# Optimization experiments

Measured on AMD Instinct MI355X. Metric: run time of the kernel, lower is better.

The kernel has to match this reference:

```python
import jax, jax.numpy as jnp
import numpy as np

N_NODES = 100000
D = 128
N_ETYPES = 4
E_PER_TYPE = 400000


def setup_inputs() -> dict:
    key = jax.random.key(0)
    k_h, k_src, k_dst, k_w = jax.random.split(key, 4)
    h = jax.random.normal(k_h, (N_NODES, D), dtype=jnp.float32)
    src = jax.random.randint(k_src, (N_ETYPES, E_PER_TYPE), 0, N_NODES, dtype=jnp.int32)
    dst = jax.random.randint(k_dst, (N_ETYPES, E_PER_TYPE), 0, N_NODES, dtype=jnp.int32)
    # Linear(2*D, 1) with xavier_uniform init
    bound = float(np.sqrt(6.0 / (2 * D + 1)))
    W_weight = jax.random.uniform(k_w, (1, 2 * D), dtype=jnp.float32,
                                  minval=-bound, maxval=bound)
    W_bias = jnp.zeros((1,), dtype=jnp.float32)
    return {"h": h, "src": src, "dst": dst, "W_weight": W_weight, "W_bias": W_bias}


def reference(h, src, dst, W_weight, W_bias):
    # Per edge type: gather src/dst node feats, concat, shared Linear(2D->1), sigmoid.
    # cat([h_u, h_v]) @ W.T == h_u @ Wu.T + h_v @ Wv.T (avoids materializing the concat).
    d = h.shape[1]
    Wu = W_weight[:, :d]   # [1, D]
    Wv = W_weight[:, d:]   # [1, D]
    h_u = h[src]           # [T, E, D] gather (irregular access)
    h_v = h[dst]           # [T, E, D]
    score = jnp.einsum('ted,od->teo', h_u, Wu) \
          + jnp.einsum('ted,od->teo', h_v, Wv) + W_bias  # [T, E, 1]
    s = jax.nn.sigmoid(score)
    # scores dict entries are the per-etype slices s[t]; s_l = concat over etypes
    return s.reshape(-1, 1)
```

## Files before the change

kernel.cpp:

```cpp
#include <hip/hip_runtime.h>
#include <math.h>

#define NODES   100000
#define DIM     128
#define NEDGES  1600000

#define LOG2E 1.44269504088896340736f

typedef int   v4i __attribute__((ext_vector_type(4)));
typedef float v4f __attribute__((ext_vector_type(4)));

__global__ __launch_bounds__(256) void node_proj_kernel(
    const float* __restrict__ h,
    const float* __restrict__ W,
    const float* __restrict__ bias_ptr,
    float* __restrict__ pu,
    float* __restrict__ pv,
    int n_nodes)
{
    int tid  = blockIdx.x * blockDim.x + threadIdx.x;
    int lane = tid & 31;
    int node = tid >> 5;
    if (node >= n_nodes) return;

    const v4f hv = __builtin_nontemporal_load(
        reinterpret_cast<const v4f*>(h + (size_t)node * DIM + lane * 4));
    const v4f wu = *reinterpret_cast<const v4f*>(W + lane * 4);
    const v4f wv = *reinterpret_cast<const v4f*>(W + DIM + lane * 4);

    float su = hv.x * wu.x + hv.y * wu.y + hv.z * wu.z + hv.w * wu.w;
    float sv = hv.x * wv.x + hv.y * wv.y + hv.z * wv.z + hv.w * wv.w;

    #pragma unroll
    for (int off = 16; off >= 1; off >>= 1) {
        su += __shfl_xor(su, off);
        sv += __shfl_xor(sv, off);
    }

    if (lane == 0) {
        pu[node] = su;
        pv[node] = sv + bias_ptr[0];
    }
}

__global__ __launch_bounds__(256) void edge_score_kernel(
    const int*   __restrict__ src,
    const int*   __restrict__ dst,
    const float* __restrict__ pu,
    const float* __restrict__ pv,
    float* __restrict__ out,
    int n_quads)
{
    int i = blockIdx.x * blockDim.x + threadIdx.x;
    if (i >= n_quads) return;

    v4i s4 = __builtin_nontemporal_load(reinterpret_cast<const v4i*>(src) + i);
    v4i d4 = __builtin_nontemporal_load(reinterpret_cast<const v4i*>(dst) + i);

    float a0 = pu[s4.x], b0 = pv[d4.x];
    float a1 = pu[s4.y], b1 = pv[d4.y];
    float a2 = pu[s4.z], b2 = pv[d4.z];
    float a3 = pu[s4.w], b3 = pv[d4.w];

    v4f r;
    r.x = a0 + b0;
    r.y = a1 + b1;
    r.z = a2 + b2;
    r.w = a3 + b3;

    r.x = __builtin_amdgcn_rcpf(1.0f + __builtin_amdgcn_exp2f(-r.x * LOG2E));
    r.y = __builtin_amdgcn_rcpf(1.0f + __builtin_amdgcn_exp2f(-r.y * LOG2E));
    r.z = __builtin_amdgcn_rcpf(1.0f + __builtin_amdgcn_exp2f(-r.z * LOG2E));
    r.w = __builtin_amdgcn_rcpf(1.0f + __builtin_amdgcn_exp2f(-r.w * LOG2E));

    __builtin_nontemporal_store(r, reinterpret_cast<v4f*>(out) + i);
}

extern "C" void kernel_launch(void* const* d_in, const int* in_sizes, int n_in,
                              void* d_out, int out_size, void* d_ws, size_t ws_size,
                              hipStream_t stream) {
    const float* h    = (const float*)d_in[0];
    const int*   src  = (const int*)d_in[1];
    const int*   dst  = (const int*)d_in[2];
    const float* W    = (const float*)d_in[3];
    const float* bias = (const float*)d_in[4];
    float* out = (float*)d_out;

    float* pu = (float*)d_ws;
    float* pv = pu + NODES;

    {
        int threads = 256;
        int total   = NODES * 32;
        int blocks  = (total + threads - 1) / threads;
        node_proj_kernel<<<blocks, threads, 0, stream>>>(h, W, bias, pu, pv, NODES);
    }

    {
        int threads = 256;
        int n_quads = NEDGES / 4;
        int blocks  = (n_quads + threads - 1) / threads;
        edge_score_kernel<<<blocks, threads, 0, stream>>>(src, dst, pu, pv, out, n_quads);
    }
}
```

Before: 33.20 us.

## Fuse node projection and edge scoring into one cooperative persistent kernel

Replaces the two kernel launches with a single cooperative kernel of 1024 blocks. Each thread prefetches its src/dst index quads before the node-projection sweep, a grid-wide sync follows, and the edge gathers and sigmoid run afterwards. The aim is to remove the launch gap between kernels and to hide the index-load latency behind the projection work. In exchange it pays for a grid barrier and the cooperative-launch overhead, and it relies on all 1024 blocks being co-resident, which a cooperative launch requires.

```diff
diff --git a/kernel.cpp b/kernel.cpp
--- a/kernel.cpp
+++ b/kernel.cpp
@@ -1,79 +1,101 @@
 #include <hip/hip_runtime.h>
-#include <math.h>
+#include <hip/hip_cooperative_groups.h>
+
+namespace cg = cooperative_groups;
 
 #define NODES   100000
 #define DIM     128
 #define NEDGES  1600000
+#define NQUADS  (NEDGES / 4)
 
 #define LOG2E 1.44269504088896340736f
+
+#define NBLK  1024
+#define NTHR  256
+#define TOTAL (NBLK * NTHR)
+#define NODES_PER_SWEEP (TOTAL / 32)
 
 typedef int   v4i __attribute__((ext_vector_type(4)));
 typedef float v4f __attribute__((ext_vector_type(4)));
 
-__global__ __launch_bounds__(256) void node_proj_kernel(
+__device__ __forceinline__ float fast_sigmoid(float x) {
+    return __builtin_amdgcn_rcpf(1.0f + __builtin_amdgcn_exp2f(-x * LOG2E));
+}
+
+__global__ __launch_bounds__(NTHR, 4) void fused_kernel(
     const float* __restrict__ h,
+    const int*   __restrict__ src,
+    const int*   __restrict__ dst,
     const float* __restrict__ W,
     const float* __restrict__ bias_ptr,
     float* __restrict__ pu,
     float* __restrict__ pv,
-    int n_nodes)
+    float* __restrict__ out)
 {
-    int tid  = blockIdx.x * blockDim.x + threadIdx.x;
-    int lane = tid & 31;
-    int node = tid >> 5;
-    if (node >= n_nodes) return;
+    const int tid  = blockIdx.x * NTHR + threadIdx.x;
+    const int lane = threadIdx.x & 31;
 
-    const v4f hv = __builtin_nontemporal_load(
-        reinterpret_cast<const v4f*>(h + (size_t)node * DIM + lane * 4));
     const v4f wu = *reinterpret_cast<const v4f*>(W + lane * 4);
     const v4f wv = *reinterpret_cast<const v4f*>(W + DIM + lane * 4);
+    const float b = bias_ptr[0];
 
-    float su = hv.x * wu.x + hv.y * wu.y + hv.z * wu.z + hv.w * wu.w;
-    float sv = hv.x * wv.x + hv.y * wv.y + hv.z * wv.z + hv.w * wv.w;
-
-    #pragma unroll
-    for (int off = 16; off >= 1; off >>= 1) {
-        su += __shfl_xor(su, off);
-        sv += __shfl_xor(sv, off);
+    const int i0 = tid;
+    const int i1 = tid + TOTAL;
+    v4i s0_ = __builtin_nontemporal_load(reinterpret_cast<const v4i*>(src) + i0);
+    v4i d0_ = __builtin_nontemporal_load(reinterpret_cast<const v4i*>(dst) + i0);
+    v4i s1_{}, d1_{};
+    const bool has1 = (i1 < NQUADS);
+    if (has1) {
+        s1_ = __builtin_nontemporal_load(reinterpret_cast<const v4i*>(src) + i1);
+        d1_ = __builtin_nontemporal_load(reinterpret_cast<const v4i*>(dst) + i1);
     }
 
-    if (lane == 0) {
-        pu[node] = su;
-        pv[node] = sv + bias_ptr[0];
+    #pragma unroll 2
+    for (int n = tid >> 5; n < NODES; n += NODES_PER_SWEEP) {
+        const v4f hv = __builtin_nontemporal_load(
+            reinterpret_cast<const v4f*>(h + (size_t)n * DIM + lane * 4));
+
+        float su = hv.x * wu.x + hv.y * wu.y + hv.z * wu.z + hv.w * wu.w;
+        float sv = hv.x * wv.x + hv.y * wv.y + hv.z * wv.z + hv.w * wv.w;
+
+        #pragma unroll
+        for (int off = 16; off >= 1; off >>= 1) {
+            su += __shfl_xor(su, off);
+            sv += __shfl_xor(sv, off);
+        }
+
+        if (lane == 0) {
+            pu[n] = su;
+            pv[n] = sv + b;
+        }
     }
-}
 
-__global__ __launch_bounds__(256) void edge_score_kernel(
-    const int*   __restrict__ src,
-    const int*   __restrict__ dst,
-    const float* __restrict__ pu,
-    const float* __restrict__ pv,
-    float* __restrict__ out,
-    int n_quads)
-{
-    int i = blockIdx.x * blockDim.x + threadIdx.x;
-    if (i >= n_quads) return;
+    cg::this_grid().sync();
 
-    v4i s4 = __builtin_nontemporal_load(reinterpret_cast<const v4i*>(src) + i);
-    v4i d4 = __builtin_nontemporal_load(reinterpret_cast<const v4i*>(dst) + i);
-
-    float a0 = pu[s4.x], b0 = pv[d4.x];
-    float a1 = pu[s4.y], b1 = pv[d4.y];
-    float a2 = pu[s4.z], b2 = pv[d4.z];
-    float a3 = pu[s4.w], b3 = pv[d4.w];
-
-    v4f r;
-    r.x = a0 + b0;
-    r.y = a1 + b1;
-    r.z = a2 + b2;
-    r.w = a3 + b3;
-
-    r.x = __builtin_amdgcn_rcpf(1.0f + __builtin_amdgcn_exp2f(-r.x * LOG2E));
-    r.y = __builtin_amdgcn_rcpf(1.0f + __builtin_amdgcn_exp2f(-r.y * LOG2E));
-    r.z = __builtin_amdgcn_rcpf(1.0f + __builtin_amdgcn_exp2f(-r.z * LOG2E));
-    r.w = __builtin_amdgcn_rcpf(1.0f + __builtin_amdgcn_exp2f(-r.w * LOG2E));
-
-    __builtin_nontemporal_store(r, reinterpret_cast<v4f*>(out) + i);
+    {
+        float a0 = pu[s0_.x], c0 = pv[d0_.x];
+        float a1 = pu[s0_.y], c1 = pv[d0_.y];
+        float a2 = pu[s0_.z], c2 = pv[d0_.z];
+        float a3 = pu[s0_.w], c3 = pv[d0_.w];
+        v4f r;
+        r.x = fast_sigmoid(a0 + c0);
+        r.y = fast_sigmoid(a1 + c1);
+        r.z = fast_sigmoid(a2 + c2);
+        r.w = fast_sigmoid(a3 + c3);
+        __builtin_nontemporal_store(r, reinterpret_cast<v4f*>(out) + i0);
+    }
+    if (has1) {
+        float a0 = pu[s1_.x], c0 = pv[d1_.x];
+        float a1 = pu[s1_.y], c1 = pv[d1_.y];
+        float a2 = pu[s1_.z], c2 = pv[d1_.z];
+        float a3 = pu[s1_.w], c3 = pv[d1_.w];
+        v4f r;
+        r.x = fast_sigmoid(a0 + c0);
+        r.y = fast_sigmoid(a1 + c1);
+        r.z = fast_sigmoid(a2 + c2);
+        r.w = fast_sigmoid(a3 + c3);
+        __builtin_nontemporal_store(r, reinterpret_cast<v4f*>(out) + i1);
+    }
 }
 
 extern "C" void kernel_launch(void* const* d_in, const int* in_sizes, int n_in,
@@ -89,17 +111,10 @@
     float* pu = (float*)d_ws;
     float* pv = pu + NODES;
 
-    {
-        int threads = 256;
-        int total   = NODES * 32;
-        int blocks  = (total + threads - 1) / threads;
-        node_proj_kernel<<<blocks, threads, 0, stream>>>(h, W, bias, pu, pv, NODES);
-    }
-
-    {
-        int threads = 256;
-        int n_quads = NEDGES / 4;
-        int blocks  = (n_quads + threads - 1) / threads;
-        edge_score_kernel<<<blocks, threads, 0, stream>>>(src, dst, pu, pv, out, n_quads);
-    }
+    void* args[] = {
+        (void*)&h, (void*)&src, (void*)&dst, (void*)&W, (void*)&bias,
+        (void*)&pu, (void*)&pv, (void*)&out
+    };
+    hipLaunchCooperativeKernel((const void*)fused_kernel,
+                               dim3(NBLK), dim3(NTHR), args, 0, stream);
 }
```

After: 118.8 us. 3.58x slower.
